# Performance work log

Hardware: AMD Instinct MI355X
Metric: run time of the kernel (lower is better)

The kernel has to match this reference:

```python
import jax, jax.numpy as jnp
import numpy as np

XX_DIM = 36
XY_DIM = 10


def setup_inputs() -> dict:
    key = jax.random.key(0)
    k_u, k_p = jax.random.split(key)
    u = jax.random.normal(k_u, (131072, XX_DIM * (XY_DIM + 1)), dtype=jnp.float32)
    # param = (F, h, c, b), canonical two-scale Lorenz96 values
    param = jnp.asarray([8.0, 1.0, 10.0, 10.0], dtype=jnp.float32)
    return {"t": 0, "u": u, "param": param}


def reference(t, u, param):
    bs = u.shape[:-1]
    F, h, c, b = param[0], param[1], param[2], param[3]
    x = u[..., :XX_DIM]                                   # [..., 36] slow vars
    y = u[..., XX_DIM:].reshape(*bs, XX_DIM, XY_DIM)      # [..., 36, 10] fast vars
    # index_select with (i+1)%n == roll(-1); (i-2)%n == roll(+2); (i-1)%n == roll(+1)
    dx = (jnp.roll(x, -1, axis=-1) - jnp.roll(x, 2, axis=-1)) * jnp.roll(x, 1, axis=-1) \
         - x + F - h * c * jnp.mean(y, axis=-1)
    dy = c * (-b * jnp.roll(y, -1, axis=-1) * (jnp.roll(y, -2, axis=-1) - jnp.roll(y, 1, axis=-1))
              - y + (h / XY_DIM) * x[..., None])
    return jnp.concatenate([dx, dy.reshape(*bs, XX_DIM * XY_DIM)], axis=-1)
```

## Files before the change

kernel.cpp:

```cpp
#include <hip/hip_runtime.h>

#define XX 36
#define XY 10
#define ROW 396
#define RPB 4
#define BLK 256
#define EPB (RPB * ROW)
#define RV4 (ROW / 4)

typedef float f4 __attribute__((ext_vector_type(4)));

#define WAVE_LDS_FENCE() asm volatile("s_waitcnt lgkmcnt(0)" ::: "memory")

__global__ __launch_bounds__(BLK, 8)
void lorenz96_fs_kernel(const float* __restrict__ u,
                        const float* __restrict__ param,
                        float* __restrict__ out) {
    __shared__ float si[EPB];
    __shared__ float so[EPB];

    const int tid = threadIdx.x;
    const int w   = tid >> 6;
    const int l   = tid & 63;

    const float F = param[0];
    const float h = param[1];
    const float c = param[2];
    const float b = param[3];

    const long long rowg = (long long)blockIdx.x * RPB + w;
    const long long gbase = rowg * ROW;

    const f4* __restrict__ in4 = (const f4*)(u + gbase);
    f4* si4 = (f4*)(si + w * ROW);
    si4[l] = in4[l];
    if (l < RV4 - 64) si4[l + 64] = in4[l + 64];

    WAVE_LDS_FENCE();

    if (l < XX) {
        const int i = l;
        const float* __restrict__ row  = si + w * ROW;
        float*       __restrict__ orow = so + w * ROW;

        const float xi  = row[i];
        const float xp1 = row[(i + 1 < XX) ? i + 1 : i + 1 - XX];
        const float xm1 = row[(i >= 1) ? i - 1 : i + XX - 1];
        const float xm2 = row[(i >= 2) ? i - 2 : i + XX - 2];

        float y[XY];
        const float* __restrict__ yr = row + XX + i * XY;
        #pragma unroll
        for (int j = 0; j < XY; ++j) y[j] = yr[j];

        float sum = 0.0f;
        #pragma unroll
        for (int j = 0; j < XY; ++j) sum += y[j];

        orow[i] = (xp1 - xm2) * xm1 - xi + F - (h * c * 0.1f) * sum;

        const float add = h * 0.1f * xi;
        const float cb  = c * b;
        float* __restrict__ oyr = orow + XX + i * XY;
        #pragma unroll
        for (int j = 0; j < XY; ++j) {
            const int jp1 = (j + 1) % XY;
            const int jp2 = (j + 2) % XY;
            const int jm1 = (j + XY - 1) % XY;
            oyr[j] = c * (add - y[j]) - cb * y[jp1] * (y[jp2] - y[jm1]);
        }
    }

    WAVE_LDS_FENCE();

    const f4* __restrict__ so4 = (const f4*)(so + w * ROW);
    f4* __restrict__ o4 = (f4*)(out + gbase);
    __builtin_nontemporal_store(so4[l], &o4[l]);
    if (l < RV4 - 64) __builtin_nontemporal_store(so4[l + 64], &o4[l + 64]);
}

extern "C" void kernel_launch(void* const* d_in, const int* in_sizes, int n_in,
                              void* d_out, int out_size, void* d_ws, size_t ws_size,
                              hipStream_t stream) {
    const float* u     = (const float*)d_in[1];
    const float* param = (const float*)d_in[2];
    float* out         = (float*)d_out;

    const int nrows   = in_sizes[1] / ROW;
    const int nblocks = nrows / RPB;

    lorenz96_fs_kernel<<<nblocks, BLK, 0, stream>>>(u, param, out);
}
```

Before: 64.83 us.

## Persistent blocks with register-prefetched tile loop over rows

Switches from one block per four rows to a fixed grid of 2048 blocks that each loop over 16 four-row tiles. The next tile's global loads go into registers while the current tile is computed and stored, overlapping load latency with compute. Row count and grid size are now hardcoded to the test shape, which drops generality for other input sizes. It also reduces the number of blocks launched.

```diff
diff --git a/kernel.cpp b/kernel.cpp
--- a/kernel.cpp
+++ b/kernel.cpp
@@ -7,6 +7,10 @@
 #define BLK 256
 #define EPB (RPB * ROW)
 #define RV4 (ROW / 4)
+#define NBLK 2048
+#define NROWS 131072
+#define NTILES (NROWS / RPB)
+#define TPB (NTILES / NBLK)
 
 typedef float f4 __attribute__((ext_vector_type(4)));
 
@@ -22,61 +26,73 @@
     const int tid = threadIdx.x;
     const int w   = tid >> 6;
     const int l   = tid & 63;
+    const bool second = (l < RV4 - 64);
 
     const float F = param[0];
     const float h = param[1];
     const float c = param[2];
     const float b = param[3];
 
-    const long long rowg = (long long)blockIdx.x * RPB + w;
-    const long long gbase = rowg * ROW;
+    const long long rbase = ((long long)blockIdx.x * TPB * RPB + w) * ROW;
+    const float* __restrict__ uw = u   + rbase;
+    float*       __restrict__ ow = out + rbase;
 
-    const f4* __restrict__ in4 = (const f4*)(u + gbase);
     f4* si4 = (f4*)(si + w * ROW);
-    si4[l] = in4[l];
-    if (l < RV4 - 64) si4[l + 64] = in4[l + 64];
+    const f4* so4 = (const f4*)(so + w * ROW);
 
-    WAVE_LDS_FENCE();
+    f4 r0 = ((const f4*)uw)[l];
+    f4 r1 = {0.f, 0.f, 0.f, 0.f};
+    if (second) r1 = ((const f4*)uw)[l + 64];
 
-    if (l < XX) {
-        const int i = l;
-        const float* __restrict__ row  = si + w * ROW;
-        float*       __restrict__ orow = so + w * ROW;
+    for (int t = 0; t < TPB; ++t) {
+        si4[l] = r0;
+        if (second) si4[l + 64] = r1;
+        WAVE_LDS_FENCE();
 
-        const float xi  = row[i];
-        const float xp1 = row[(i + 1 < XX) ? i + 1 : i + 1 - XX];
-        const float xm1 = row[(i >= 1) ? i - 1 : i + XX - 1];
-        const float xm2 = row[(i >= 2) ? i - 2 : i + XX - 2];
+        if (t + 1 < TPB) {
+            const f4* nxt = (const f4*)(uw + (long long)(t + 1) * EPB);
+            r0 = nxt[l];
+            if (second) r1 = nxt[l + 64];
+        }
 
-        float y[XY];
-        const float* __restrict__ yr = row + XX + i * XY;
-        #pragma unroll
-        for (int j = 0; j < XY; ++j) y[j] = yr[j];
+        if (l < XX) {
+            const int i = l;
+            const float* __restrict__ row  = si + w * ROW;
+            float*       __restrict__ orow = so + w * ROW;
 
-        float sum = 0.0f;
-        #pragma unroll
-        for (int j = 0; j < XY; ++j) sum += y[j];
+            const float xi  = row[i];
+            const float xp1 = row[(i + 1 < XX) ? i + 1 : i + 1 - XX];
+            const float xm1 = row[(i >= 1) ? i - 1 : i + XX - 1];
+            const float xm2 = row[(i >= 2) ? i - 2 : i + XX - 2];
 
-        orow[i] = (xp1 - xm2) * xm1 - xi + F - (h * c * 0.1f) * sum;
+            float y[XY];
+            const float* __restrict__ yr = row + XX + i * XY;
+            #pragma unroll
+            for (int j = 0; j < XY; ++j) y[j] = yr[j];
 
-        const float add = h * 0.1f * xi;
-        const float cb  = c * b;
-        float* __restrict__ oyr = orow + XX + i * XY;
-        #pragma unroll
-        for (int j = 0; j < XY; ++j) {
-            const int jp1 = (j + 1) % XY;
-            const int jp2 = (j + 2) % XY;
-            const int jm1 = (j + XY - 1) % XY;
-            oyr[j] = c * (add - y[j]) - cb * y[jp1] * (y[jp2] - y[jm1]);
+            float sum = 0.0f;
+            #pragma unroll
+            for (int j = 0; j < XY; ++j) sum += y[j];
+
+            orow[i] = (xp1 - xm2) * xm1 - xi + F - (h * c * 0.1f) * sum;
+
+            const float add = h * 0.1f * xi;
+            const float cb  = c * b;
+            float* __restrict__ oyr = orow + XX + i * XY;
+            #pragma unroll
+            for (int j = 0; j < XY; ++j) {
+                const int jp1 = (j + 1) % XY;
+                const int jp2 = (j + 2) % XY;
+                const int jm1 = (j + XY - 1) % XY;
+                oyr[j] = c * (add - y[j]) - cb * y[jp1] * (y[jp2] - y[jm1]);
+            }
         }
+        WAVE_LDS_FENCE();
+
+        f4* __restrict__ o4 = (f4*)(ow + (long long)t * EPB);
+        __builtin_nontemporal_store(so4[l], &o4[l]);
+        if (second) __builtin_nontemporal_store(so4[l + 64], &o4[l + 64]);
     }
-
-    WAVE_LDS_FENCE();
-
-    const f4* __restrict__ so4 = (const f4*)(so + w * ROW);
-    f4* __restrict__ o4 = (f4*)(out + gbase);
-    __builtin_nontemporal_store(so4[l], &o4[l]);
-    if (l < RV4 - 64) __builtin_nontemporal_store(so4[l + 64], &o4[l + 64]);
 }
 
 extern "C" void kernel_launch(void* const* d_in, const int* in_sizes, int n_in,
@@ -86,8 +102,5 @@
     const float* param = (const float*)d_in[2];
     float* out         = (float*)d_out;
 
-    const int nrows   = in_sizes[1] / ROW;
-    const int nblocks = nrows / RPB;
-
-    lorenz96_fs_kernel<<<nblocks, BLK, 0, stream>>>(u, param, out);
+    lorenz96_fs_kernel<<<NBLK, BLK, 0, stream>>>(u, param, out);
 }
```

Result: slower. 68.78 us (+6.1%).
